# Performance work log

Measured on AMD Instinct MI355X. Metric: run time of the kernel, lower is better.

The kernel has to match this reference:

```python
import jax, jax.numpy as jnp
import numpy as np

N, K, T, M, P = 16, 256, 1000, 384, 2
BN_EPS = 1e-3  # keras BatchNormalization default


def setup_inputs() -> dict:
    key = jax.random.key(0)
    ks = jax.random.split(key, 16)
    inp = {
        "V": jax.random.normal(ks[0], (N, K, M), dtype=jnp.float32),
        "duration_outputs": jax.random.normal(ks[1], (N, K), dtype=jnp.float32) * 0.5,
        # ConvBatchNorm params (Conv1D(8, kernel=3, same) + BN, inference mode)
        "conv_w": jax.random.normal(ks[2], (3, M, 8), dtype=jnp.float32) * 0.05,
        "conv_b": jnp.zeros((8,), dtype=jnp.float32),
        "bn_gamma": jnp.ones((8,), dtype=jnp.float32),
        "bn_beta": jnp.zeros((8,), dtype=jnp.float32),
        "bn_mean": jnp.zeros((8,), dtype=jnp.float32),
        "bn_var": jnp.ones((8,), dtype=jnp.float32),
        # score MLP: 10 -> 16 -> 16 -> 1
        "w1": jax.random.normal(ks[3], (10, 16), dtype=jnp.float32) * 0.3,
        "b1": jnp.zeros((16,), dtype=jnp.float32),
        "w2": jax.random.normal(ks[4], (16, 16), dtype=jnp.float32) * 0.25,
        "b2": jnp.zeros((16,), dtype=jnp.float32),
        "w3": jax.random.normal(ks[5], (16, 1), dtype=jnp.float32) * 0.25,
        "b3": jnp.zeros((1,), dtype=jnp.float32),
        # auxiliary MLP: 10 -> P -> P
        "aw1": jax.random.normal(ks[6], (10, P), dtype=jnp.float32) * 0.3,
        "ab1": jnp.zeros((P,), dtype=jnp.float32),
        "aw2": jax.random.normal(ks[7], (P, P), dtype=jnp.float32) * 0.5,
        "ab2": jnp.zeros((P,), dtype=jnp.float32),
        # projection P -> M (no bias)
        "proj_w": jax.random.normal(ks[8], (P, M), dtype=jnp.float32) * 0.05,
        "max_mel_length": T,
    }
    return inp


def _forward(V, duration_outputs, conv_w, conv_b, bn_gamma, bn_beta, bn_mean,
             bn_var, w1, b1, w2, b2, w3, b3, aw1, ab1, aw2, ab2, proj_w,
             max_mel_length):
    silu = jax.nn.silu
    # durations and start/end boundaries
    durations = jax.nn.relu(jnp.exp(duration_outputs) - 1.0)      # [N,K]
    S = jnp.cumsum(durations, axis=1) - durations                 # exclusive cumsum [N,K]
    E = S + durations                                             # [N,K]
    tgrid = jnp.arange(1, max_mel_length + 1, dtype=V.dtype)      # [T]
    S_mat = tgrid[None, :, None] - S[:, None, :]                  # [N,T,K]
    E_mat = E[:, None, :] - tgrid[None, :, None]                  # [N,T,K]
    # ConvBatchNorm on V (inference: BN uses moving stats, dropout is no-op)
    conv = jax.lax.conv_general_dilated(
        V, conv_w, window_strides=(1,), padding='SAME',
        dimension_numbers=('NWC', 'WIO', 'NWC')) + conv_b         # [N,K,8]
    conv = (conv - bn_mean) * jax.lax.rsqrt(bn_var + BN_EPS) * bn_gamma + bn_beta
    conv_V = silu(conv)                                           # [N,K,8]
    n, t, k = S_mat.shape
    conv_b4 = jnp.broadcast_to(conv_V[:, None, :, :], (n, t, k, conv_V.shape[-1]))
    W_input = jnp.concatenate(
        [S_mat[..., None], E_mat[..., None], conv_b4], axis=-1)   # [N,T,K,10]
    # score MLP + softmax over K
    h = silu(W_input @ w1 + b1)
    h = silu(h @ w2 + b2)
    score = (h @ w3 + b3)[..., 0]                                 # [N,T,K]
    W = jax.nn.softmax(score, axis=-1)
    # auxiliary MLP and weighted reduction
    C = silu(silu(W_input @ aw1 + ab1) @ aw2 + ab2)               # [N,T,K,P]
    proj_C = jnp.einsum('ntk,ntkp->ntp', W, C) @ proj_w           # [N,T,M]
    O = jnp.einsum('ntk,nkm->ntm', W, V) + proj_C                 # [N,T,M]
    return O


def reference(V, duration_outputs, conv_w, conv_b, bn_gamma, bn_beta, bn_mean,
              bn_var, w1, b1, w2, b2, w3, b3, aw1, ab1, aw2, ab2, proj_w,
              max_mel_length):
    return _forward(V, duration_outputs, conv_w, conv_b, bn_gamma, bn_beta,
                    bn_mean, bn_var, w1, b1, w2, b2, w3, b3, aw1, ab1, aw2,
                    ab2, proj_w, max_mel_length)
```

## Files before the change

### kernel.cpp

```cpp
#include <hip/hip_runtime.h>

#define NN 16
#define KK 256
#define TT 1000
#define MM 384
#define TCH 16
#define TOB 28
#define TP 1008
#define TPAD 1024

typedef short bf16x8 __attribute__((ext_vector_type(8)));
typedef float f32x4 __attribute__((ext_vector_type(4)));

__device__ __forceinline__ float fast_rcp(float x) { return __builtin_amdgcn_rcpf(x); }
__device__ __forceinline__ float silu_f(float x) {
    float e = __expf(-x);
    return x * fast_rcp(1.0f + e);
}
__device__ __forceinline__ unsigned short f2bf_rne(float f) {
    unsigned u = __float_as_uint(f);
    unsigned r = u + 0x7fff + ((u >> 16) & 1);
    return (unsigned short)(r >> 16);
}
__device__ __forceinline__ float bf2f(unsigned short h) {
    return __uint_as_float((unsigned)h << 16);
}

__global__ void k_scan(const float* __restrict__ dur_out,
                       float* __restrict__ wsS, float* __restrict__ wsD) {
    __shared__ float lds[KK];
    int n = blockIdx.x, k = threadIdx.x;
    float d = __expf(dur_out[n * KK + k]) - 1.0f;
    d = fmaxf(d, 0.0f);
    lds[k] = d;
    __syncthreads();
    float run = d;
    for (int off = 1; off < KK; off <<= 1) {
        float v = (k >= off) ? lds[k - off] : 0.0f;
        __syncthreads();
        run += v;
        lds[k] = run;
        __syncthreads();
    }
    wsS[n * KK + k] = run - d;
    wsD[n * KK + k] = d;
}

__global__ __launch_bounds__(256) void k_conv(
    const float* __restrict__ V, const float* __restrict__ conv_w,
    const float* __restrict__ conv_b, const float* __restrict__ bn_g,
    const float* __restrict__ bn_b, const float* __restrict__ bn_m,
    const float* __restrict__ bn_v, const float* __restrict__ w1,
    const float* __restrict__ b1, const float* __restrict__ aw1,
    const float* __restrict__ ab1, const float* __restrict__ wsD,
    float* __restrict__ wsQ1, float* __restrict__ wsQA) {
    __shared__ float wt[8 * 3 * MM];
    int tid = threadIdx.x;
    int n = blockIdx.y;
    for (int i = tid; i < 3 * MM * 8; i += 256) {
        int tap = i / (MM * 8);
        int r = i - tap * (MM * 8);
        int m = r >> 3, c = r & 7;
        wt[(c * 3 + tap) * MM + m] = conv_w[i];
    }
    __syncthreads();

    int wv = tid >> 6, lane = tid & 63;
    int k = blockIdx.x * 4 + wv;
    const float* Vn = V + (size_t)n * KK * MM;

    float p[8];
#pragma unroll
    for (int c = 0; c < 8; ++c) p[c] = 0.f;

#pragma unroll
    for (int tap = 0; tap < 3; ++tap) {
        int kk = k + tap - 1;
        if (kk < 0 || kk >= KK) continue;
        const float* vrow = Vn + (size_t)kk * MM;
#pragma unroll
        for (int j = 0; j < 6; ++j) {
            int m = lane + 64 * j;
            float v = vrow[m];
#pragma unroll
            for (int c = 0; c < 8; ++c)
                p[c] = fmaf(v, wt[(c * 3 + tap) * MM + m], p[c]);
        }
    }
#pragma unroll
    for (int c = 0; c < 8; ++c) {
#pragma unroll
        for (int off = 32; off >= 1; off >>= 1) p[c] += __shfl_xor(p[c], off);
    }
    float cv[8];
#pragma unroll
    for (int c = 0; c < 8; ++c) {
        float xx = p[c] + conv_b[c];
        float bn = (xx - bn_m[c]) * (bn_g[c] * rsqrtf(bn_v[c] + 1e-3f)) + bn_b[c];
        cv[c] = silu_f(bn);
    }
    float d = wsD[n * KK + k];
    if (lane < 16) {
        int j = lane;
        float q = fmaf(d, w1[16 + j], b1[j]);
#pragma unroll
        for (int c = 0; c < 8; ++c) q = fmaf(cv[c], w1[(2 + c) * 16 + j], q);
        wsQ1[((size_t)(n * KK + k)) * 16 + j] = q;
    } else if (lane < 18) {
        int pp = lane - 16;
        float q = fmaf(d, aw1[2 + pp], ab1[pp]);
#pragma unroll
        for (int c = 0; c < 8; ++c) q = fmaf(cv[c], aw1[(2 + c) * 2 + pp], q);
        wsQA[(size_t)(n * KK + k) * 2 + pp] = q;
    }
}

__global__ __launch_bounds__(256) void k_vt(
    const float* __restrict__ V, unsigned short* __restrict__ Vth,
    unsigned short* __restrict__ Vtl) {
    __shared__ float tile[64][65];
    int m0 = blockIdx.x * 64, k0 = blockIdx.y * 64, n = blockIdx.z;
    int tid = threadIdx.x;
    const float* Vn = V + (size_t)n * KK * MM;
    int mo = tid & 63, ks = tid >> 6;
    for (int kk = ks; kk < 64; kk += 4)
        tile[kk][mo] = Vn[(size_t)(k0 + kk) * MM + m0 + mo];
    __syncthreads();
    int ko = tid & 63, ms = tid >> 6;
    for (int mm = ms; mm < 64; mm += 4) {
        float v = tile[ko][mm];
        unsigned short hi = f2bf_rne(v);
        unsigned short lo = f2bf_rne(v - bf2f(hi));
        size_t o = ((size_t)n * MM + m0 + mm) * KK + k0 + ko;
        Vth[o] = hi;
        Vtl[o] = lo;
    }
}

__global__ __launch_bounds__(256) void k_score(
    const float* __restrict__ w1, const float* __restrict__ w2g,
    const float* __restrict__ b2g, const float* __restrict__ w3g,
    const float* __restrict__ b3g, const float* __restrict__ aw1,
    const float* __restrict__ aw2g, const float* __restrict__ ab2g,
    const float* __restrict__ wsS, const float* __restrict__ wsQ1,
    const float* __restrict__ wsQA, float* __restrict__ wcg,
    float* __restrict__ ETf, unsigned short* __restrict__ ETh,
    unsigned short* __restrict__ ETl, int use_bf16) {
    __shared__ __align__(16) float sc[TCH * KK];
    __shared__ __align__(16) float rl[16];

    int tid = threadIdx.x;
    int tb = blockIdx.x * TCH;
    int n = blockIdx.y;
    int nK = n * KK;

    if (tid < 16) rl[tid] = w1[tid] - w1[16 + tid];

    float b3v = b3g[0];
    int k = tid;
    float S_k = wsS[nK + k];
    float q1[16];
    {
        const float4* q1p = (const float4*)&wsQ1[(size_t)(nK + k) * 16];
#pragma unroll
        for (int g = 0; g < 4; ++g) {
            float4 qv = q1p[g];
            q1[4 * g + 0] = qv.x; q1[4 * g + 1] = qv.y;
            q1[4 * g + 2] = qv.z; q1[4 * g + 3] = qv.w;
        }
    }
    __syncthreads();

    for (int tq = 0; tq < TCH / 4; ++tq) {
        float s0 = (float)(tb + 4 * tq + 1) - S_k;
        float aA[16], aB[16], aC[16], aD[16];
#pragma unroll
        for (int j = 0; j < 16; ++j) { aA[j] = 0.f; aB[j] = 0.f; aC[j] = 0.f; aD[j] = 0.f; }
#pragma unroll
        for (int j1 = 0; j1 < 16; ++j1) {
            float r = rl[j1];
            float q = q1[j1];
            float hA = silu_f(fmaf(s0, r, q));
            float hB = silu_f(fmaf(s0 + 1.0f, r, q));
            float hC = silu_f(fmaf(s0 + 2.0f, r, q));
            float hD = silu_f(fmaf(s0 + 3.0f, r, q));
            const float4* wr = (const float4*)&w2g[j1 * 16];
#pragma unroll
            for (int g = 0; g < 4; ++g) {
                float4 w = wr[g];
                aA[4 * g + 0] = fmaf(hA, w.x, aA[4 * g + 0]);
                aA[4 * g + 1] = fmaf(hA, w.y, aA[4 * g + 1]);
                aA[4 * g + 2] = fmaf(hA, w.z, aA[4 * g + 2]);
                aA[4 * g + 3] = fmaf(hA, w.w, aA[4 * g + 3]);
                aB[4 * g + 0] = fmaf(hB, w.x, aB[4 * g + 0]);
                aB[4 * g + 1] = fmaf(hB, w.y, aB[4 * g + 1]);
                aB[4 * g + 2] = fmaf(hB, w.z, aB[4 * g + 2]);
                aB[4 * g + 3] = fmaf(hB, w.w, aB[4 * g + 3]);
                aC[4 * g + 0] = fmaf(hC, w.x, aC[4 * g + 0]);
                aC[4 * g + 1] = fmaf(hC, w.y, aC[4 * g + 1]);
                aC[4 * g + 2] = fmaf(hC, w.z, aC[4 * g + 2]);
                aC[4 * g + 3] = fmaf(hC, w.w, aC[4 * g + 3]);
                aD[4 * g + 0] = fmaf(hD, w.x, aD[4 * g + 0]);
                aD[4 * g + 1] = fmaf(hD, w.y, aD[4 * g + 1]);
                aD[4 * g + 2] = fmaf(hD, w.z, aD[4 * g + 2]);
                aD[4 * g + 3] = fmaf(hD, w.w, aD[4 * g + 3]);
            }
        }
        float scA = b3v, scB = b3v, scC = b3v, scD = b3v;
#pragma unroll
        for (int g = 0; g < 4; ++g) {
            float4 bq = *(const float4*)&b2g[4 * g];
            float4 wq = *(const float4*)&w3g[4 * g];
            scA += silu_f(aA[4 * g + 0] + bq.x) * wq.x + silu_f(aA[4 * g + 1] + bq.y) * wq.y +
                   silu_f(aA[4 * g + 2] + bq.z) * wq.z + silu_f(aA[4 * g + 3] + bq.w) * wq.w;
            scB += silu_f(aB[4 * g + 0] + bq.x) * wq.x + silu_f(aB[4 * g + 1] + bq.y) * wq.y +
                   silu_f(aB[4 * g + 2] + bq.z) * wq.z + silu_f(aB[4 * g + 3] + bq.w) * wq.w;
            scC += silu_f(aC[4 * g + 0] + bq.x) * wq.x + silu_f(aC[4 * g + 1] + bq.y) * wq.y +
                   silu_f(aC[4 * g + 2] + bq.z) * wq.z + silu_f(aC[4 * g + 3] + bq.w) * wq.w;
            scD += silu_f(aD[4 * g + 0] + bq.x) * wq.x + silu_f(aD[4 * g + 1] + bq.y) * wq.y +
                   silu_f(aD[4 * g + 2] + bq.z) * wq.z + silu_f(aD[4 * g + 3] + bq.w) * wq.w;
        }
        sc[(4 * tq + 0) * KK + k] = scA;
        sc[(4 * tq + 1) * KK + k] = scB;
        sc[(4 * tq + 2) * KK + k] = scC;
        sc[(4 * tq + 3) * KK + k] = scD;
    }
    __syncthreads();

    {
        float rA0 = aw1[0] - aw1[2];
        float rA1 = aw1[1] - aw1[3];
        float aw200 = aw2g[0], aw201 = aw2g[1], aw210 = aw2g[2], aw211 = aw2g[3];
        float ab20 = ab2g[0], ab21 = ab2g[1];
        int wv = tid >> 6, lane = tid & 63;
        float S4[4]; float2 QA4[4];
#pragma unroll
        for (int j = 0; j < 4; ++j) {
            int kk2 = lane + 64 * j;
            S4[j] = wsS[nK + kk2];
            QA4[j] = *(const float2*)&wsQA[(size_t)(nK + kk2) * 2];
        }
#pragma unroll
        for (int i = 0; i < 4; ++i) {
            int t = wv * 4 + i;
            int tt = tb + t;
            float v0 = sc[t * KK + lane];
            float v1 = sc[t * KK + lane + 64];
            float v2 = sc[t * KK + lane + 128];
            float v3 = sc[t * KK + lane + 192];
            float mx = fmaxf(fmaxf(v0, v1), fmaxf(v2, v3));
#pragma unroll
            for (int off = 32; off >= 1; off >>= 1) mx = fmaxf(mx, __shfl_xor(mx, off));
            float e0 = __expf(v0 - mx), e1 = __expf(v1 - mx);
            float e2 = __expf(v2 - mx), e3 = __expf(v3 - mx);
            float ssum = e0 + e1 + e2 + e3;
            float wc0 = 0.f, wc1 = 0.f;
            float tc = (float)(tt + 1);
            float ear[4] = {e0, e1, e2, e3};
#pragma unroll
            for (int j = 0; j < 4; ++j) {
                float s = tc - S4[j];
                float a0 = silu_f(fmaf(s, rA0, QA4[j].x));
                float a1 = silu_f(fmaf(s, rA1, QA4[j].y));
                float c0 = silu_f(fmaf(a1, aw210, fmaf(a0, aw200, ab20)));
                float c1 = silu_f(fmaf(a1, aw211, fmaf(a0, aw201, ab21)));
                wc0 = fmaf(ear[j], c0, wc0);
                wc1 = fmaf(ear[j], c1, wc1);
            }
#pragma unroll
            for (int off = 32; off >= 1; off >>= 1) {
                ssum += __shfl_xor(ssum, off);
                wc0 += __shfl_xor(wc0, off);
                wc1 += __shfl_xor(wc1, off);
            }
            float inv = fast_rcp(ssum);
            sc[t * KK + lane]       = e0 * inv;
            sc[t * KK + lane + 64]  = e1 * inv;
            sc[t * KK + lane + 128] = e2 * inv;
            sc[t * KK + lane + 192] = e3 * inv;
            if (lane == 0 && tt < TT) {
                wcg[(size_t)(n * TT + tt) * 2]     = wc0 * inv;
                wcg[(size_t)(n * TT + tt) * 2 + 1] = wc1 * inv;
            }
        }
    }
    __syncthreads();

    if (use_bf16) {
#pragma unroll
        for (int t2 = 0; t2 < TCH; ++t2) {
            float e = sc[t2 * KK + k];
            unsigned short hi = f2bf_rne(e);
            unsigned short lo = f2bf_rne(e - bf2f(hi));
            size_t o = ((size_t)n * TPAD + tb + t2) * KK + k;
            ETh[o] = hi;
            ETl[o] = lo;
        }
    } else {
        for (int idx = tid; idx < TCH * KK; idx += 256) {
            int k2 = idx >> 4, t2 = idx & 15;
            if (tb + t2 < TT)
                ETf[((size_t)(nK + k2)) * TP + tb + t2] = sc[t2 * KK + k2];
        }
    }
}

__global__ __launch_bounds__(384) void k_gemm(
    const unsigned short* __restrict__ ETh, const unsigned short* __restrict__ ETl,
    const unsigned short* __restrict__ Vth, const unsigned short* __restrict__ Vtl,
    const float* __restrict__ wcg, const float* __restrict__ projw,
    float* __restrict__ out) {
    int tid = threadIdx.x;
    int w = tid >> 6, lane = tid & 63;
    int tb = blockIdx.x * 32;
    int n = blockIdx.y;
    int r16 = lane & 15, kh = lane >> 4;
    int mb = w * 64;

    const unsigned short* eh0 = ETh + ((size_t)n * TPAD + tb + r16) * KK + kh * 8;
    const unsigned short* el0 = ETl + ((size_t)n * TPAD + tb + r16) * KK + kh * 8;
    const unsigned short* vh0 = Vth + ((size_t)n * MM + mb + r16) * KK + kh * 8;
    const unsigned short* vl0 = Vtl + ((size_t)n * MM + mb + r16) * KK + kh * 8;

    f32x4 acc[2][4];
#pragma unroll
    for (int tt = 0; tt < 2; ++tt)
#pragma unroll
        for (int mm = 0; mm < 4; ++mm) acc[tt][mm] = (f32x4){0.f, 0.f, 0.f, 0.f};

#pragma unroll
    for (int kb = 0; kb < 8; ++kb) {
        int ko = kb * 32;
        bf16x8 ah0 = *(const bf16x8*)(eh0 + ko);
        bf16x8 ah1 = *(const bf16x8*)(eh0 + 16 * KK + ko);
        bf16x8 al0 = *(const bf16x8*)(el0 + ko);
        bf16x8 al1 = *(const bf16x8*)(el0 + 16 * KK + ko);
#pragma unroll
        for (int mm = 0; mm < 4; ++mm) {
            bf16x8 bh = *(const bf16x8*)(vh0 + (size_t)mm * 16 * KK + ko);
            bf16x8 bl = *(const bf16x8*)(vl0 + (size_t)mm * 16 * KK + ko);
            acc[0][mm] = __builtin_amdgcn_mfma_f32_16x16x32_bf16(ah0, bh, acc[0][mm], 0, 0, 0);
            acc[0][mm] = __builtin_amdgcn_mfma_f32_16x16x32_bf16(ah0, bl, acc[0][mm], 0, 0, 0);
            acc[0][mm] = __builtin_amdgcn_mfma_f32_16x16x32_bf16(al0, bh, acc[0][mm], 0, 0, 0);
            acc[1][mm] = __builtin_amdgcn_mfma_f32_16x16x32_bf16(ah1, bh, acc[1][mm], 0, 0, 0);
            acc[1][mm] = __builtin_amdgcn_mfma_f32_16x16x32_bf16(ah1, bl, acc[1][mm], 0, 0, 0);
            acc[1][mm] = __builtin_amdgcn_mfma_f32_16x16x32_bf16(al1, bh, acc[1][mm], 0, 0, 0);
        }
    }

#pragma unroll
    for (int tt = 0; tt < 2; ++tt) {
#pragma unroll
        for (int r = 0; r < 4; ++r) {
            int t = tb + tt * 16 + kh * 4 + r;
            if (t < TT) {
                float c0 = wcg[(size_t)(n * TT + t) * 2];
                float c1 = wcg[(size_t)(n * TT + t) * 2 + 1];
#pragma unroll
                for (int mm = 0; mm < 4; ++mm) {
                    int m = mb + mm * 16 + r16;
                    float pw0 = projw[m], pw1 = projw[MM + m];
                    out[((size_t)n * TT + t) * MM + m] =
                        acc[tt][mm][r] + c0 * pw0 + c1 * pw1;
                }
            }
        }
    }
}

__global__ __launch_bounds__(384) void k_out(
    const float* __restrict__ V, const float* __restrict__ projw,
    const float* __restrict__ wcg, const float* __restrict__ ET,
    float* __restrict__ out) {
    int tid = threadIdx.x;
    int tb = blockIdx.x * TOB;
    int n = blockIdx.y;
    int nK = n * KK;
    const float* Vn = V + (size_t)n * KK * MM;
    const float* Eb = ET + (size_t)nK * TP + tb;
    int m = tid;

    float acc[TOB];
#pragma unroll
    for (int t = 0; t < TOB; ++t) acc[t] = 0.f;

    for (int kx = 0; kx < KK; ++kx) {
        const float4* ep = (const float4*)(Eb + (size_t)kx * TP);
        float vv = Vn[(size_t)kx * MM + m];
#pragma unroll
        for (int q = 0; q < TOB / 4; ++q) {
            float4 e = ep[q];
            acc[4 * q + 0] = fmaf(e.x, vv, acc[4 * q + 0]);
            acc[4 * q + 1] = fmaf(e.y, vv, acc[4 * q + 1]);
            acc[4 * q + 2] = fmaf(e.z, vv, acc[4 * q + 2]);
            acc[4 * q + 3] = fmaf(e.w, vv, acc[4 * q + 3]);
        }
    }

    float pw0 = projw[m], pw1 = projw[MM + m];
#pragma unroll
    for (int t = 0; t < TOB; ++t) {
        int tt = tb + t;
        if (tt < TT) {
            float c0 = wcg[(size_t)(n * TT + tt) * 2];
            float c1 = wcg[(size_t)(n * TT + tt) * 2 + 1];
            out[((size_t)n * TT + tt) * MM + m] = acc[t] + c0 * pw0 + c1 * pw1;
        }
    }
}

extern "C" void kernel_launch(void* const* d_in, const int* in_sizes, int n_in,
                              void* d_out, int out_size, void* d_ws, size_t ws_size,
                              hipStream_t stream) {
    const float* V   = (const float*)d_in[0];
    const float* dur = (const float*)d_in[1];
    const float* cw  = (const float*)d_in[2];
    const float* cb  = (const float*)d_in[3];
    const float* bng = (const float*)d_in[4];
    const float* bnb = (const float*)d_in[5];
    const float* bnm = (const float*)d_in[6];
    const float* bnv = (const float*)d_in[7];
    const float* w1  = (const float*)d_in[8];
    const float* b1  = (const float*)d_in[9];
    const float* w2  = (const float*)d_in[10];
    const float* b2  = (const float*)d_in[11];
    const float* w3  = (const float*)d_in[12];
    const float* b3  = (const float*)d_in[13];
    const float* aw1 = (const float*)d_in[14];
    const float* ab1 = (const float*)d_in[15];
    const float* aw2 = (const float*)d_in[16];
    const float* ab2 = (const float*)d_in[17];
    const float* pw  = (const float*)d_in[18];
    float* out = (float*)d_out;
    float* ws = (float*)d_ws;

    float* wsS  = ws;
    float* wsD  = ws + 4096;
    float* wsQ1 = ws + 8192;
    float* wsQA = ws + 73728;
    float* wcg  = ws + 81920;
    char*  base = (char*)(ws + 114688);

    size_t sz_ETh = (size_t)NN * TPAD * KK * 2;
    size_t sz_Vt  = (size_t)NN * MM * KK * 2;
    size_t need   = 114688 * 4 + 2 * sz_ETh + 2 * sz_Vt;
    bool mfma_path = (ws_size >= need);

    hipLaunchKernelGGL(k_scan, dim3(NN), dim3(KK), 0, stream, dur, wsS, wsD);
    hipLaunchKernelGGL(k_conv, dim3(KK / 4, NN), dim3(256), 0, stream, V, cw, cb,
                       bng, bnb, bnm, bnv, w1, b1, aw1, ab1, wsD, wsQ1, wsQA);

    if (mfma_path) {
        unsigned short* ETh = (unsigned short*)base;
        unsigned short* ETl = (unsigned short*)(base + sz_ETh);
        unsigned short* Vth = (unsigned short*)(base + 2 * sz_ETh);
        unsigned short* Vtl = (unsigned short*)(base + 2 * sz_ETh + sz_Vt);
        hipLaunchKernelGGL(k_vt, dim3(MM / 64, KK / 64, NN), dim3(256), 0, stream,
                           V, Vth, Vtl);
        hipLaunchKernelGGL(k_score, dim3((TT + TCH - 1) / TCH, NN), dim3(256), 0,
                           stream, w1, w2, b2, w3, b3, aw1, aw2, ab2, wsS, wsQ1,
                           wsQA, wcg, (float*)nullptr, ETh, ETl, 1);
        hipLaunchKernelGGL(k_gemm, dim3(TPAD / 32, NN), dim3(384), 0, stream,
                           ETh, ETl, Vth, Vtl, wcg, pw, out);
    } else {
        float* ETf = (float*)base;
        hipLaunchKernelGGL(k_score, dim3((TT + TCH - 1) / TCH, NN), dim3(256), 0,
                           stream, w1, w2, b2, w3, b3, aw1, aw2, ab2, wsS, wsQ1,
                           wsQA, wcg, ETf, (unsigned short*)nullptr,
                           (unsigned short*)nullptr, 0);
        hipLaunchKernelGGL(k_out, dim3((TT + TOB - 1) / TOB, NN), dim3(384), 0,
                           stream, V, pw, wcg, ETf, out);
    }
}
```

Before: 143.4 us.

## Merge scan and V-transpose kernels; stage ET tile in LDS with 12-wave GEMM blocks

New measurement: 151.4 us. 1.06x slower.

```diff
diff --git a/kernel.cpp b/kernel.cpp
--- a/kernel.cpp
+++ b/kernel.cpp
@@ -26,24 +26,49 @@
     return __uint_as_float((unsigned)h << 16);
 }
 
-__global__ void k_scan(const float* __restrict__ dur_out,
-                       float* __restrict__ wsS, float* __restrict__ wsD) {
-    __shared__ float lds[KK];
-    int n = blockIdx.x, k = threadIdx.x;
-    float d = __expf(dur_out[n * KK + k]) - 1.0f;
-    d = fmaxf(d, 0.0f);
-    lds[k] = d;
-    __syncthreads();
-    float run = d;
-    for (int off = 1; off < KK; off <<= 1) {
-        float v = (k >= off) ? lds[k - off] : 0.0f;
+__global__ __launch_bounds__(256) void k_init(
+    const float* __restrict__ dur_out, float* __restrict__ wsS,
+    float* __restrict__ wsD, const float* __restrict__ V,
+    unsigned short* __restrict__ Vth, unsigned short* __restrict__ Vtl) {
+    int tid = threadIdx.x;
+    if (blockIdx.x < 16) {
+        __shared__ float lds[KK];
+        int n = blockIdx.x, k = tid;
+        float d = __expf(dur_out[n * KK + k]) - 1.0f;
+        d = fmaxf(d, 0.0f);
+        lds[k] = d;
         __syncthreads();
-        run += v;
-        lds[k] = run;
+        float run = d;
+        for (int off = 1; off < KK; off <<= 1) {
+            float v = (k >= off) ? lds[k - off] : 0.0f;
+            __syncthreads();
+            run += v;
+            lds[k] = run;
+            __syncthreads();
+        }
+        wsS[n * KK + k] = run - d;
+        wsD[n * KK + k] = d;
+    } else {
+        __shared__ float tile[64][65];
+        int id = blockIdx.x - 16;
+        int m0 = (id % 6) * 64;
+        int k0 = ((id / 6) & 3) * 64;
+        int n = id / 24;
+        const float* Vn = V + (size_t)n * KK * MM;
+        int mo = tid & 63, ks = tid >> 6;
+        for (int kk = ks; kk < 64; kk += 4)
+            tile[kk][mo] = Vn[(size_t)(k0 + kk) * MM + m0 + mo];
         __syncthreads();
-    }
-    wsS[n * KK + k] = run - d;
-    wsD[n * KK + k] = d;
+        int ko = tid & 63, ms = tid >> 6;
+        for (int mm = ms; mm < 64; mm += 4) {
+            float v = tile[ko][mm];
+            unsigned short hi = f2bf_rne(v);
+            unsigned short lo = f2bf_rne(v - bf2f(hi));
+            size_t o = ((size_t)n * MM + m0 + mm) * KK + k0 + ko;
+            Vth[o] = hi;
+            Vtl[o] = lo;
+        }
+    }
 }
 
 __global__ __launch_bounds__(256) void k_conv(
@@ -112,28 +137,6 @@
 #pragma unroll
         for (int c = 0; c < 8; ++c) q = fmaf(cv[c], aw1[(2 + c) * 2 + pp], q);
         wsQA[(size_t)(n * KK + k) * 2 + pp] = q;
-    }
-}
-
-__global__ __launch_bounds__(256) void k_vt(
-    const float* __restrict__ V, unsigned short* __restrict__ Vth,
-    unsigned short* __restrict__ Vtl) {
-    __shared__ float tile[64][65];
-    int m0 = blockIdx.x * 64, k0 = blockIdx.y * 64, n = blockIdx.z;
-    int tid = threadIdx.x;
-    const float* Vn = V + (size_t)n * KK * MM;
-    int mo = tid & 63, ks = tid >> 6;
-    for (int kk = ks; kk < 64; kk += 4)
-        tile[kk][mo] = Vn[(size_t)(k0 + kk) * MM + m0 + mo];
-    __syncthreads();
-    int ko = tid & 63, ms = tid >> 6;
-    for (int mm = ms; mm < 64; mm += 4) {
-        float v = tile[ko][mm];
-        unsigned short hi = f2bf_rne(v);
-        unsigned short lo = f2bf_rne(v - bf2f(hi));
-        size_t o = ((size_t)n * MM + m0 + mm) * KK + k0 + ko;
-        Vth[o] = hi;
-        Vtl[o] = lo;
     }
 }
 
@@ -305,64 +308,71 @@
     }
 }
 
-__global__ __launch_bounds__(384) void k_gemm(
+__global__ __launch_bounds__(768) void k_gemm(
     const unsigned short* __restrict__ ETh, const unsigned short* __restrict__ ETl,
     const unsigned short* __restrict__ Vth, const unsigned short* __restrict__ Vtl,
     const float* __restrict__ wcg, const float* __restrict__ projw,
     float* __restrict__ out) {
+    __shared__ __align__(16) char eh_l[32 * 512];
+    __shared__ __align__(16) char el_l[32 * 512];
     int tid = threadIdx.x;
     int w = tid >> 6, lane = tid & 63;
     int tb = blockIdx.x * 32;
     int n = blockIdx.y;
+
+    for (int i = tid; i < 2048; i += 768) {
+        int buf = i >> 10;
+        int r = (i >> 5) & 31, c = i & 31;
+        int byte = r * 512 + c * 16;
+        int swz = byte ^ ((r & 7) << 4);
+        const unsigned short* src = (buf ? ETl : ETh) +
+            ((size_t)(n * TPAD + tb + r)) * KK + c * 8;
+        char* dst = (buf ? el_l : eh_l) + swz;
+        *(int4*)dst = *(const int4*)src;
+    }
+    __syncthreads();
+
     int r16 = lane & 15, kh = lane >> 4;
-    int mb = w * 64;
-
-    const unsigned short* eh0 = ETh + ((size_t)n * TPAD + tb + r16) * KK + kh * 8;
-    const unsigned short* el0 = ETl + ((size_t)n * TPAD + tb + r16) * KK + kh * 8;
+    int ts = (w & 1) * 16;
+    int mb = (w >> 1) * 64;
+    int arow = ts + r16;
+    int abase = arow * 512;
+    int aswz = (arow & 7) << 4;
+
     const unsigned short* vh0 = Vth + ((size_t)n * MM + mb + r16) * KK + kh * 8;
     const unsigned short* vl0 = Vtl + ((size_t)n * MM + mb + r16) * KK + kh * 8;
 
-    f32x4 acc[2][4];
-#pragma unroll
-    for (int tt = 0; tt < 2; ++tt)
-#pragma unroll
-        for (int mm = 0; mm < 4; ++mm) acc[tt][mm] = (f32x4){0.f, 0.f, 0.f, 0.f};
+    f32x4 acc[4];
+#pragma unroll
+    for (int mm = 0; mm < 4; ++mm) acc[mm] = (f32x4){0.f, 0.f, 0.f, 0.f};
 
 #pragma unroll
     for (int kb = 0; kb < 8; ++kb) {
+        int off = abase + ((kb * 64 + kh * 16) ^ aswz);
+        bf16x8 ah = *(const bf16x8*)(eh_l + off);
+        bf16x8 al = *(const bf16x8*)(el_l + off);
         int ko = kb * 32;
-        bf16x8 ah0 = *(const bf16x8*)(eh0 + ko);
-        bf16x8 ah1 = *(const bf16x8*)(eh0 + 16 * KK + ko);
-        bf16x8 al0 = *(const bf16x8*)(el0 + ko);
-        bf16x8 al1 = *(const bf16x8*)(el0 + 16 * KK + ko);
 #pragma unroll
         for (int mm = 0; mm < 4; ++mm) {
             bf16x8 bh = *(const bf16x8*)(vh0 + (size_t)mm * 16 * KK + ko);
             bf16x8 bl = *(const bf16x8*)(vl0 + (size_t)mm * 16 * KK + ko);
-            acc[0][mm] = __builtin_amdgcn_mfma_f32_16x16x32_bf16(ah0, bh, acc[0][mm], 0, 0, 0);
-            acc[0][mm] = __builtin_amdgcn_mfma_f32_16x16x32_bf16(ah0, bl, acc[0][mm], 0, 0, 0);
-            acc[0][mm] = __builtin_amdgcn_mfma_f32_16x16x32_bf16(al0, bh, acc[0][mm], 0, 0, 0);
-            acc[1][mm] = __builtin_amdgcn_mfma_f32_16x16x32_bf16(ah1, bh, acc[1][mm], 0, 0, 0);
-            acc[1][mm] = __builtin_amdgcn_mfma_f32_16x16x32_bf16(ah1, bl, acc[1][mm], 0, 0, 0);
-            acc[1][mm] = __builtin_amdgcn_mfma_f32_16x16x32_bf16(al1, bh, acc[1][mm], 0, 0, 0);
-        }
-    }
-
-#pragma unroll
-    for (int tt = 0; tt < 2; ++tt) {
-#pragma unroll
-        for (int r = 0; r < 4; ++r) {
-            int t = tb + tt * 16 + kh * 4 + r;
-            if (t < TT) {
-                float c0 = wcg[(size_t)(n * TT + t) * 2];
-                float c1 = wcg[(size_t)(n * TT + t) * 2 + 1];
-#pragma unroll
-                for (int mm = 0; mm < 4; ++mm) {
-                    int m = mb + mm * 16 + r16;
-                    float pw0 = projw[m], pw1 = projw[MM + m];
-                    out[((size_t)n * TT + t) * MM + m] =
-                        acc[tt][mm][r] + c0 * pw0 + c1 * pw1;
-                }
+            acc[mm] = __builtin_amdgcn_mfma_f32_16x16x32_bf16(ah, bh, acc[mm], 0, 0, 0);
+            acc[mm] = __builtin_amdgcn_mfma_f32_16x16x32_bf16(ah, bl, acc[mm], 0, 0, 0);
+            acc[mm] = __builtin_amdgcn_mfma_f32_16x16x32_bf16(al, bh, acc[mm], 0, 0, 0);
+        }
+    }
+
+#pragma unroll
+    for (int r = 0; r < 4; ++r) {
+        int t = tb + ts + kh * 4 + r;
+        if (t < TT) {
+            float c0 = wcg[(size_t)(n * TT + t) * 2];
+            float c1 = wcg[(size_t)(n * TT + t) * 2 + 1];
+#pragma unroll
+            for (int mm = 0; mm < 4; ++mm) {
+                int m = mb + mm * 16 + r16;
+                float pw0 = projw[m], pw1 = projw[MM + m];
+                out[((size_t)n * TT + t) * MM + m] = acc[mm][r] + c0 * pw0 + c1 * pw1;
             }
         }
     }
@@ -446,24 +456,29 @@
     size_t need   = 114688 * 4 + 2 * sz_ETh + 2 * sz_Vt;
     bool mfma_path = (ws_size >= need);
 
-    hipLaunchKernelGGL(k_scan, dim3(NN), dim3(KK), 0, stream, dur, wsS, wsD);
-    hipLaunchKernelGGL(k_conv, dim3(KK / 4, NN), dim3(256), 0, stream, V, cw, cb,
-                       bng, bnb, bnm, bnv, w1, b1, aw1, ab1, wsD, wsQ1, wsQA);
-
     if (mfma_path) {
         unsigned short* ETh = (unsigned short*)base;
         unsigned short* ETl = (unsigned short*)(base + sz_ETh);
         unsigned short* Vth = (unsigned short*)(base + 2 * sz_ETh);
         unsigned short* Vtl = (unsigned short*)(base + 2 * sz_ETh + sz_Vt);
-        hipLaunchKernelGGL(k_vt, dim3(MM / 64, KK / 64, NN), dim3(256), 0, stream,
-                           V, Vth, Vtl);
+        hipLaunchKernelGGL(k_init, dim3(16 + 6 * 4 * NN), dim3(256), 0, stream,
+                           dur, wsS, wsD, V, Vth, Vtl);
+        hipLaunchKernelGGL(k_conv, dim3(KK / 4, NN), dim3(256), 0, stream, V, cw,
+                           cb, bng, bnb, bnm, bnv, w1, b1, aw1, ab1, wsD, wsQ1,
+                           wsQA);
         hipLaunchKernelGGL(k_score, dim3((TT + TCH - 1) / TCH, NN), dim3(256), 0,
                            stream, w1, w2, b2, w3, b3, aw1, aw2, ab2, wsS, wsQ1,
                            wsQA, wcg, (float*)nullptr, ETh, ETl, 1);
-        hipLaunchKernelGGL(k_gemm, dim3(TPAD / 32, NN), dim3(384), 0, stream,
+        hipLaunchKernelGGL(k_gemm, dim3(TPAD / 32, NN), dim3(768), 0, stream,
                            ETh, ETl, Vth, Vtl, wcg, pw, out);
     } else {
         float* ETf = (float*)base;
+        hipLaunchKernelGGL(k_init, dim3(16), dim3(256), 0, stream,
+                           dur, wsS, wsD, V, (unsigned short*)nullptr,
+                           (unsigned short*)nullptr);
+        hipLaunchKernelGGL(k_conv, dim3(KK / 4, NN), dim3(256), 0, stream, V, cw,
+                           cb, bng, bnb, bnm, bnv, w1, b1, aw1, ab1, wsD, wsQ1,
+                           wsQA);
         hipLaunchKernelGGL(k_score, dim3((TT + TCH - 1) / TCH, NN), dim3(256), 0,
                            stream, w1, w2, b2, w3, b3, aw1, aw2, ab2, wsS, wsQ1,
                            wsQA, wcg, ETf, (unsigned short*)nullptr,
```
